# Optimization experiments

Measured on AMD Instinct MI355X. Metric: run time of the kernel, lower is better.

The kernel has to match this reference:

```python
import jax, jax.numpy as jnp
import numpy as np

N, D, E, C = 100000, 256, 262144, 5


def setup_inputs() -> dict:
    key = jax.random.key(0)
    ks = jax.random.split(key, 8)
    s = 1.0 / np.sqrt(D)
    return {
        "node_feat": jax.random.normal(ks[0], (N, D), jnp.float32),
        "pair_idx": jax.random.randint(ks[1], (E, 2), 0, N, dtype=jnp.int64)
        if jax.config.jax_enable_x64 else jax.random.randint(ks[1], (E, 2), 0, N, dtype=jnp.int32),
        "W_agg": jax.random.normal(ks[2], (2 * D, D), jnp.float32) * (1.0 / np.sqrt(2 * D)),
        "b_agg": jnp.zeros((D,), jnp.float32),
        "We1": jax.random.normal(ks[3], (D, D), jnp.float32) * s,
        "be1": jnp.zeros((D,), jnp.float32),
        "We2": jax.random.normal(ks[4], (D, C), jnp.float32) * s,
        "be2": jnp.zeros((C,), jnp.float32),
        "Wn1": jax.random.normal(ks[5], (D, D), jnp.float32) * s,
        "bn1": jnp.zeros((D,), jnp.float32),
        "Wn2": jax.random.normal(ks[6], (D, 2), jnp.float32) * s,
        "bn2": jnp.zeros((2,), jnp.float32),
    }


def reference(node_feat, pair_idx, W_agg, b_agg, We1, be1, We2, be2, Wn1, bn1, Wn2, bn2):
    # node_predictor: Linear -> ReLU -> Linear (D -> D -> 2)
    node_res = jnp.maximum(node_feat @ Wn1 + bn1, 0.0) @ Wn2 + bn2  # [N, 2]

    # gather node-pair features for both directed orderings (x,y) and (y,x)
    src = node_feat[pair_idx[:, 0]]  # [E, D]
    dst = node_feat[pair_idx[:, 1]]  # [E, D]
    # edge_feat_agger(cat(src,dst)) + edge_feat_agger(cat(dst,src))
    ef_fwd = jnp.concatenate([src, dst], axis=-1) @ W_agg + b_agg  # [E, D]
    ef_bwd = jnp.concatenate([dst, src], axis=-1) @ W_agg + b_agg  # [E, D]
    ed_feat = ef_fwd + ef_bwd

    # edge_predictor: Linear -> ReLU -> Linear (D -> D -> C)
    pred_edge = jnp.maximum(ed_feat @ We1 + be1, 0.0) @ We2 + be2  # [E, C]
    return node_res, pred_edge
```

## Files before the change

kernel.cpp:

```cpp
#include <hip/hip_runtime.h>

#define D 256

typedef float f32x4 __attribute__((ext_vector_type(4)));
typedef short short8 __attribute__((ext_vector_type(8)));
typedef __bf16 bf16x8 __attribute__((ext_vector_type(8)));

static __device__ __forceinline__ short f2bs(float f) {
    __bf16 b = (__bf16)f;
    return __builtin_bit_cast(short, b);
}
static __device__ __forceinline__ float bs2f(short s) {
    unsigned u = ((unsigned)(unsigned short)s) << 16;
    return __builtin_bit_cast(float, u);
}


__global__ void pre_bc(const float* __restrict__ b_agg, const float* __restrict__ We1,
                       const float* __restrict__ be1, float* __restrict__ bc)
{
    int j = threadIdx.x;
    float acc = be1[j];
    for (int k = 0; k < D; ++k)
        acc += 2.f * b_agg[k] * We1[k * D + j];
    bc[j] = acc;
}

__global__ void pre_wct(const float* __restrict__ W_agg, const float* __restrict__ We1,
                        short* __restrict__ WcT)
{
    __shared__ float wsrow[D];
    int i = blockIdx.x, j = threadIdx.x;
    wsrow[j] = W_agg[i * D + j] + W_agg[(i + D) * D + j];
    __syncthreads();
    float acc = 0.f;
    for (int k = 0; k < D; ++k)
        acc += wsrow[k] * We1[k * D + j];
    WcT[j * D + i] = f2bs(acc);
}

__global__ void pre_wn1t(const float* __restrict__ Wn1, short* __restrict__ Wn1T)
{
    int i = blockIdx.x, j = threadIdx.x;
    Wn1T[j * D + i] = f2bs(Wn1[i * D + j]);
}

__global__ void pre_w2t(const float* __restrict__ We2, const float* __restrict__ Wn2,
                        short* __restrict__ We2T, short* __restrict__ Wn2T)
{
    int k = threadIdx.x;
    for (int c = 0; c < 16; ++c) {
        float ve = (c < 5) ? We2[k * 5 + c] : 0.f;
        float vn = (c < 2) ? Wn2[k * 2 + c] : 0.f;
        We2T[c * D + k] = f2bs(ve);
        Wn2T[c * D + k] = f2bs(vn);
    }
}

__global__ __launch_bounds__(512, 4)
void node_h_gemm(const float* __restrict__ nf,
                 const short* __restrict__ WcT, const short* __restrict__ Wn1T,
                 const float* __restrict__ bc,  const float* __restrict__ bn1,
                 const short* __restrict__ Wn2T, const float* __restrict__ bn2,
                 short* __restrict__ H, float* __restrict__ outn, int nrows)
{
    __shared__ __align__(16) short sA[64 * D];
    __shared__ __align__(16) short hl[64 * D];

    const int tid = threadIdx.x;
    const int lane = tid & 63;
    const int w = tid >> 6;
    const int l15 = lane & 15;
    const int g = lane >> 4;
    const int rowblk = blockIdx.x * 64;

    {
        const int row = tid >> 3;
        const int q = tid & 7;
        int r = rowblk + row; if (r > nrows - 1) r = nrows - 1;
        const float4* p = reinterpret_cast<const float4*>(nf + (size_t)r * D + q * 32);
#pragma unroll
        for (int j = 0; j < 4; ++j) {
            float4 x0 = p[2 * j], x1 = p[2 * j + 1];
            bf16x8 v = {(__bf16)x0.x, (__bf16)x0.y, (__bf16)x0.z, (__bf16)x0.w,
                        (__bf16)x1.x, (__bf16)x1.y, (__bf16)x1.z, (__bf16)x1.w};
            const int c = q * 4 + j;
            *reinterpret_cast<short8*>(&sA[row * D + ((c ^ (row & 7)) * 8)]) =
                __builtin_bit_cast(short8, v);
        }
    }
    __syncthreads();

    const short* Wb = (w < 4) ? WcT : Wn1T;
    const int nc0 = (w & 3) * 4;

    f32x4 acc[4][4];
#pragma unroll
    for (int f = 0; f < 4; ++f)
#pragma unroll
        for (int t = 0; t < 4; ++t)
            acc[f][t] = f32x4{0.f, 0.f, 0.f, 0.f};

#pragma unroll
    for (int ks = 0; ks < 8; ++ks) {
        const int k0 = ks * 32 + g * 8;
        const int c = ks * 4 + g;
        short8 a[4];
#pragma unroll
        for (int f = 0; f < 4; ++f) {
            const int row = f * 16 + l15;
            a[f] = *reinterpret_cast<const short8*>(&sA[row * D + ((c ^ (row & 7)) * 8)]);
        }
#pragma unroll
        for (int t = 0; t < 4; ++t) {
            short8 bw = *reinterpret_cast<const short8*>(Wb + ((nc0 + t) * 16 + l15) * D + k0);
#pragma unroll
            for (int f = 0; f < 4; ++f)
                acc[f][t] = __builtin_amdgcn_mfma_f32_16x16x32_bf16(a[f], bw, acc[f][t], 0, 0, 0);
        }
    }

    __syncthreads();

    if (w < 4) {
#pragma unroll
        for (int t = 0; t < 4; ++t) {
            const int col = w * 64 + t * 16 + l15;
            const float bb = 0.5f * bc[col];
#pragma unroll
            for (int f = 0; f < 4; ++f)
#pragma unroll
                for (int r = 0; r < 4; ++r) {
                    const int row = f * 16 + g * 4 + r;
                    sA[row * D + col] = f2bs(acc[f][t][r] + bb);
                }
        }
    } else {
#pragma unroll
        for (int t = 0; t < 4; ++t) {
            const int col = (w - 4) * 64 + t * 16 + l15;
            const float bb = bn1[col];
            const int chunk = col >> 3;
#pragma unroll
            for (int f = 0; f < 4; ++f)
#pragma unroll
                for (int r = 0; r < 4; ++r) {
                    const int row = f * 16 + g * 4 + r;
                    float v = fmaxf(acc[f][t][r] + bb, 0.f);
                    hl[row * D + (((chunk ^ (row & 7)) << 3) | (col & 7))] = f2bs(v);
                }
        }
    }

    __syncthreads();

    if (w < 4) {
        const int row = w * 16 + (lane >> 2);
        const int grow = rowblk + row;
#pragma unroll
        for (int j = 0; j < 8; ++j) {
            const int ch = (lane & 3) * 8 + j;
            short8 v = *reinterpret_cast<const short8*>(&sA[row * D + ch * 8]);
            if (grow < nrows)
                *reinterpret_cast<short8*>(H + (size_t)grow * D + ch * 8) = v;
        }
    } else {
        const int vr = w - 4;
        const int row = vr * 16 + l15;
        f32x4 a2 = f32x4{0.f, 0.f, 0.f, 0.f};
#pragma unroll
        for (int ks = 0; ks < 8; ++ks) {
            const int k0 = ks * 32 + g * 8;
            const int c = ks * 4 + g;
            short8 bw = *reinterpret_cast<const short8*>(Wn2T + l15 * D + k0);
            short8 ah = *reinterpret_cast<const short8*>(&hl[row * D + ((c ^ (row & 7)) * 8)]);
            a2 = __builtin_amdgcn_mfma_f32_16x16x32_bf16(ah, bw, a2, 0, 0, 0);
        }
        if (l15 < 2) {
            const float b2 = bn2[l15];
#pragma unroll
            for (int r = 0; r < 4; ++r) {
                const int grow = rowblk + vr * 16 + g * 4 + r;
                if (grow < nrows)
                    outn[(size_t)grow * 2 + l15] = a2[r] + b2;
            }
        }
    }
}

__global__ __launch_bounds__(256, 4)
void edge_gemv(const short* __restrict__ H, const int* __restrict__ pair,
               const short* __restrict__ We2T, const float* __restrict__ be2,
               float* __restrict__ out, int nedges)
{
    const int lane = threadIdx.x & 63;
    const int w = threadIdx.x >> 6;
    const int l15 = lane & 15;
    const int g = lane >> 4;

    short8 Bf[8];
#pragma unroll
    for (int ks = 0; ks < 8; ++ks)
        Bf[ks] = *reinterpret_cast<const short8*>(We2T + l15 * D + ks * 32 + g * 8);

    const float b2 = (l15 < 5) ? be2[l15] : 0.f;
    const int base = blockIdx.x * 256 + w * 64;

#pragma unroll
    for (int grp = 0; grp < 4; ++grp) {
        int e = base + grp * 16 + l15;
        if (e > nedges - 1) e = nedges - 1;
        const size_t si = (size_t)(unsigned)pair[2 * e];
        const size_t di = (size_t)(unsigned)pair[2 * e + 1];
        const short8* sp = reinterpret_cast<const short8*>(H + si * D + g * 8);
        const short8* dp = reinterpret_cast<const short8*>(H + di * D + g * 8);
        short8 sv[8], dv[8];
#pragma unroll
        for (int ks = 0; ks < 8; ++ks) {
            sv[ks] = sp[ks * 4];
            dv[ks] = dp[ks * 4];
        }
        f32x4 acc = f32x4{0.f, 0.f, 0.f, 0.f};
#pragma unroll
        for (int ks = 0; ks < 8; ++ks) {
            short8 a;
#pragma unroll
            for (int i = 0; i < 8; ++i)
                a[i] = f2bs(fmaxf(bs2f(sv[ks][i]) + bs2f(dv[ks][i]), 0.f));
            acc = __builtin_amdgcn_mfma_f32_16x16x32_bf16(a, Bf[ks], acc, 0, 0, 0);
        }
        if (l15 < 5) {
#pragma unroll
            for (int r = 0; r < 4; ++r) {
                const int ge = base + grp * 16 + g * 4 + r;
                if (ge < nedges)
                    out[(size_t)ge * 5 + l15] = acc[r] + b2;
            }
        }
    }
}

template<int MODE>
__global__ __launch_bounds__(256, 2)
void fused_mlp(const float* __restrict__ feat,
               const int* __restrict__ pair,
               const short* __restrict__ W1T,
               const float* __restrict__ bias1,
               const short* __restrict__ W2T,
               const float* __restrict__ bias2,
               float* __restrict__ out,
               int nrows, int ncols)
{
    __shared__ short hl[128 * D];

    const int tid = threadIdx.x;
    const int lane = tid & 63;
    const int w = tid >> 6;
    const int l15 = lane & 15;
    const int g = lane >> 4;
    const int rowblk = blockIdx.x * 128 + w * 32;

    const float* ap0[2];
    const float* ap1[2];
#pragma unroll
    for (int f = 0; f < 2; ++f) {
        int r = rowblk + f * 16 + l15;
        if (r > nrows - 1) r = nrows - 1;
        if constexpr (MODE == 0) {
            ap0[f] = feat + (size_t)r * D;
            ap1[f] = nullptr;
        } else {
            ap0[f] = feat + (size_t)pair[2 * r] * D;
            ap1[f] = feat + (size_t)pair[2 * r + 1] * D;
        }
    }

    f32x4 acc[2][16];
#pragma unroll
    for (int f = 0; f < 2; ++f)
#pragma unroll
        for (int t = 0; t < 16; ++t)
            acc[f][t] = f32x4{0.f, 0.f, 0.f, 0.f};

#pragma unroll
    for (int ks = 0; ks < 8; ++ks) {
        const int k0 = ks * 32 + g * 8;
        short8 af[2];
#pragma unroll
        for (int f = 0; f < 2; ++f) {
            const float4* p0 = reinterpret_cast<const float4*>(ap0[f] + k0);
            float4 x0 = p0[0], x1 = p0[1];
            if constexpr (MODE == 1) {
                const float4* p1 = reinterpret_cast<const float4*>(ap1[f] + k0);
                float4 y0 = p1[0], y1 = p1[1];
                x0.x += y0.x; x0.y += y0.y; x0.z += y0.z; x0.w += y0.w;
                x1.x += y1.x; x1.y += y1.y; x1.z += y1.z; x1.w += y1.w;
            }
            bf16x8 bv = {(__bf16)x0.x, (__bf16)x0.y, (__bf16)x0.z, (__bf16)x0.w,
                         (__bf16)x1.x, (__bf16)x1.y, (__bf16)x1.z, (__bf16)x1.w};
            af[f] = __builtin_bit_cast(short8, bv);
        }
#pragma unroll
        for (int t = 0; t < 16; ++t) {
            short8 bw = *reinterpret_cast<const short8*>(W1T + ((t * 16 + l15) * D + k0));
            acc[0][t] = __builtin_amdgcn_mfma_f32_16x16x32_bf16(af[0], bw, acc[0][t], 0, 0, 0);
            acc[1][t] = __builtin_amdgcn_mfma_f32_16x16x32_bf16(af[1], bw, acc[1][t], 0, 0, 0);
        }
    }

#pragma unroll
    for (int t = 0; t < 16; ++t) {
        const int col = t * 16 + l15;
        const float b = bias1[col];
        const int chunk = col >> 3;
#pragma unroll
        for (int f = 0; f < 2; ++f) {
#pragma unroll
            for (int r = 0; r < 4; ++r) {
                const int rl = w * 32 + f * 16 + g * 4 + r;
                float v = fmaxf(acc[f][t][r] + b, 0.f);
                hl[rl * D + ((chunk ^ (rl & 7)) << 3) + (col & 7)] = f2bs(v);
            }
        }
    }

    __syncthreads();

    f32x4 acc2[2];
    acc2[0] = f32x4{0.f, 0.f, 0.f, 0.f};
    acc2[1] = f32x4{0.f, 0.f, 0.f, 0.f};
#pragma unroll
    for (int ks = 0; ks < 8; ++ks) {
        const int k0 = ks * 32 + g * 8;
        const int chunk = k0 >> 3;
        short8 bw = *reinterpret_cast<const short8*>(W2T + (l15 * D + k0));
#pragma unroll
        for (int f = 0; f < 2; ++f) {
            const int rl = w * 32 + f * 16 + l15;
            short8 ah = *reinterpret_cast<const short8*>(&hl[rl * D + ((chunk ^ (rl & 7)) << 3)]);
            acc2[f] = __builtin_amdgcn_mfma_f32_16x16x32_bf16(ah, bw, acc2[f], 0, 0, 0);
        }
    }

    if (l15 < ncols) {
        const float b2 = bias2[l15];
#pragma unroll
        for (int f = 0; f < 2; ++f) {
#pragma unroll
            for (int r = 0; r < 4; ++r) {
                const int grow = rowblk + f * 16 + g * 4 + r;
                if (grow < nrows)
                    out[(size_t)grow * ncols + l15] = acc2[f][r] + b2;
            }
        }
    }
}


extern "C" void kernel_launch(void* const* d_in, const int* in_sizes, int n_in,
                              void* d_out, int out_size, void* d_ws, size_t ws_size,
                              hipStream_t stream)
{
    const float* node_feat = (const float*)d_in[0];
    const int*   pair_idx  = (const int*)d_in[1];
    const float* W_agg     = (const float*)d_in[2];
    const float* b_agg     = (const float*)d_in[3];
    const float* We1       = (const float*)d_in[4];
    const float* be1       = (const float*)d_in[5];
    const float* We2       = (const float*)d_in[6];
    const float* be2       = (const float*)d_in[7];
    const float* Wn1       = (const float*)d_in[8];
    const float* bn1       = (const float*)d_in[9];
    const float* Wn2       = (const float*)d_in[10];
    const float* bn2       = (const float*)d_in[11];

    const int N = in_sizes[0] / D;
    const int E = in_sizes[1] / 2;

    float* out = (float*)d_out;
    char*  ws  = (char*)d_ws;

    short* WcT  = (short*)(ws + 0);
    short* Wn1T = (short*)(ws + 131072);
    short* We2T = (short*)(ws + 262144);
    short* Wn2T = (short*)(ws + 270336);
    float* bc   = (float*)(ws + 278528);
    const size_t H_OFF = 524288;
    short* H = (short*)(ws + H_OFF);
    const size_t need = H_OFF + (size_t)N * D * 2;

    pre_bc<<<1, 256, 0, stream>>>(b_agg, We1, be1, bc);
    pre_wct<<<D, 256, 0, stream>>>(W_agg, We1, WcT);
    pre_wn1t<<<D, 256, 0, stream>>>(Wn1, Wn1T);
    pre_w2t<<<1, 256, 0, stream>>>(We2, Wn2, We2T, Wn2T);

    if (ws_size >= need) {
        node_h_gemm<<<(N + 63) / 64, 512, 0, stream>>>(
            node_feat, WcT, Wn1T, bc, bn1, Wn2T, bn2, H, out, N);

        edge_gemv<<<(E + 255) / 256, 256, 0, stream>>>(
            H, pair_idx, We2T, be2, out + (size_t)2 * N, E);
    } else {
        fused_mlp<0><<<(N + 127) / 128, 256, 0, stream>>>(
            node_feat, nullptr, Wn1T, bn1, Wn2T, bn2, out, N, 2);

        fused_mlp<1><<<E / 128, 256, 0, stream>>>(
            node_feat, pair_idx, WcT, bc, We2T, be2, out + (size_t)2 * N, E, 5);
    }
}
```

Baseline: 174.9 us.

## Preload weight fragments into registers and stage A in MFMA fragment order

The node GEMM kernel now loads each wave's full set of weight B-fragments into registers up front, so the k-loop no longer issues global loads. The A tile is written to shared memory in MFMA fragment order, so each lane reads contiguous 16-byte chunks without an XOR swizzle. The H output is stored directly from accumulators to global memory (2-byte scattered stores), removing a shared-memory staging pass and one barrier. The occupancy hint drops from 4 to 2 blocks per SM because of the larger register footprint, and the H stores become uncoalesced.

```diff
diff --git a/kernel.cpp b/kernel.cpp
--- a/kernel.cpp
+++ b/kernel.cpp
@@ -57,14 +57,14 @@
     }
 }
 
-__global__ __launch_bounds__(512, 4)
-void node_h_gemm(const float* __restrict__ nf,
-                 const short* __restrict__ WcT, const short* __restrict__ Wn1T,
-                 const float* __restrict__ bc,  const float* __restrict__ bn1,
-                 const short* __restrict__ Wn2T, const float* __restrict__ bn2,
-                 short* __restrict__ H, float* __restrict__ outn, int nrows)
-{
-    __shared__ __align__(16) short sA[64 * D];
+__global__ __launch_bounds__(512, 2)
+void node_h_gemm2(const float* __restrict__ nf,
+                  const short* __restrict__ WcT, const short* __restrict__ Wn1T,
+                  const float* __restrict__ bc,  const float* __restrict__ bn1,
+                  const short* __restrict__ Wn2T, const float* __restrict__ bn2,
+                  short* __restrict__ H, float* __restrict__ outn, int nrows)
+{
+    __shared__ __align__(16) short sA[2048 * 8];
     __shared__ __align__(16) short hl[64 * D];
 
     const int tid = threadIdx.x;
@@ -74,25 +74,29 @@
     const int g = lane >> 4;
     const int rowblk = blockIdx.x * 64;
 
-    {
-        const int row = tid >> 3;
-        const int q = tid & 7;
-        int r = rowblk + row; if (r > nrows - 1) r = nrows - 1;
-        const float4* p = reinterpret_cast<const float4*>(nf + (size_t)r * D + q * 32);
-#pragma unroll
-        for (int j = 0; j < 4; ++j) {
-            float4 x0 = p[2 * j], x1 = p[2 * j + 1];
-            bf16x8 v = {(__bf16)x0.x, (__bf16)x0.y, (__bf16)x0.z, (__bf16)x0.w,
-                        (__bf16)x1.x, (__bf16)x1.y, (__bf16)x1.z, (__bf16)x1.w};
-            const int c = q * 4 + j;
-            *reinterpret_cast<short8*>(&sA[row * D + ((c ^ (row & 7)) * 8)]) =
-                __builtin_bit_cast(short8, v);
-        }
-    }
-    __syncthreads();
-
     const short* Wb = (w < 4) ? WcT : Wn1T;
     const int nc0 = (w & 3) * 4;
+    short8 Bw[4][8];
+#pragma unroll
+    for (int t = 0; t < 4; ++t)
+#pragma unroll
+        for (int ks = 0; ks < 8; ++ks)
+            Bw[t][ks] = *reinterpret_cast<const short8*>(
+                Wb + ((nc0 + t) * 16 + l15) * D + ks * 32 + g * 8);
+
+#pragma unroll
+    for (int j = 0; j < 4; ++j) {
+        const int i = j * 512 + tid;
+        const int li = i & 15, gi = (i >> 4) & 3, fi = (i >> 6) & 3, ki = i >> 8;
+        int r = rowblk + fi * 16 + li;
+        if (r > nrows - 1) r = nrows - 1;
+        const float4* p = reinterpret_cast<const float4*>(nf + (size_t)r * D + ki * 32 + gi * 8);
+        float4 x0 = p[0], x1 = p[1];
+        bf16x8 v = {(__bf16)x0.x, (__bf16)x0.y, (__bf16)x0.z, (__bf16)x0.w,
+                    (__bf16)x1.x, (__bf16)x1.y, (__bf16)x1.z, (__bf16)x1.w};
+        *reinterpret_cast<short8*>(&sA[i * 8]) = __builtin_bit_cast(short8, v);
+    }
+    __syncthreads();
 
     f32x4 acc[4][4];
 #pragma unroll
@@ -103,24 +107,16 @@
 
 #pragma unroll
     for (int ks = 0; ks < 8; ++ks) {
-        const int k0 = ks * 32 + g * 8;
-        const int c = ks * 4 + g;
         short8 a[4];
 #pragma unroll
-        for (int f = 0; f < 4; ++f) {
-            const int row = f * 16 + l15;
-            a[f] = *reinterpret_cast<const short8*>(&sA[row * D + ((c ^ (row & 7)) * 8)]);
-        }
-#pragma unroll
-        for (int t = 0; t < 4; ++t) {
-            short8 bw = *reinterpret_cast<const short8*>(Wb + ((nc0 + t) * 16 + l15) * D + k0);
+        for (int f = 0; f < 4; ++f)
+            a[f] = *reinterpret_cast<const short8*>(&sA[(ks * 256 + f * 64 + lane) * 8]);
+#pragma unroll
+        for (int t = 0; t < 4; ++t)
 #pragma unroll
             for (int f = 0; f < 4; ++f)
-                acc[f][t] = __builtin_amdgcn_mfma_f32_16x16x32_bf16(a[f], bw, acc[f][t], 0, 0, 0);
-        }
-    }
-
-    __syncthreads();
+                acc[f][t] = __builtin_amdgcn_mfma_f32_16x16x32_bf16(a[f], Bw[t][ks], acc[f][t], 0, 0, 0);
+    }
 
     if (w < 4) {
 #pragma unroll
@@ -131,8 +127,9 @@
             for (int f = 0; f < 4; ++f)
 #pragma unroll
                 for (int r = 0; r < 4; ++r) {
-                    const int row = f * 16 + g * 4 + r;
-                    sA[row * D + col] = f2bs(acc[f][t][r] + bb);
+                    const int grow = rowblk + f * 16 + g * 4 + r;
+                    if (grow < nrows)
+                        H[(size_t)grow * D + col] = f2bs(acc[f][t][r] + bb);
                 }
         }
     } else {
@@ -154,17 +151,7 @@
 
     __syncthreads();
 
-    if (w < 4) {
-        const int row = w * 16 + (lane >> 2);
-        const int grow = rowblk + row;
-#pragma unroll
-        for (int j = 0; j < 8; ++j) {
-            const int ch = (lane & 3) * 8 + j;
-            short8 v = *reinterpret_cast<const short8*>(&sA[row * D + ch * 8]);
-            if (grow < nrows)
-                *reinterpret_cast<short8*>(H + (size_t)grow * D + ch * 8) = v;
-        }
-    } else {
+    if (w >= 4) {
         const int vr = w - 4;
         const int row = vr * 16 + l15;
         f32x4 a2 = f32x4{0.f, 0.f, 0.f, 0.f};
@@ -395,7 +382,7 @@
     pre_w2t<<<1, 256, 0, stream>>>(We2, Wn2, We2T, Wn2T);
 
     if (ws_size >= need) {
-        node_h_gemm<<<(N + 63) / 64, 512, 0, stream>>>(
+        node_h_gemm2<<<(N + 63) / 64, 512, 0, stream>>>(
             node_feat, WcT, Wn1T, bc, bn1, Wn2T, bn2, H, out, N);
 
         edge_gemv<<<(E + 255) / 256, 256, 0, stream>>>(
```

New measurement: 168.4 us. 3.7% less time.
